# Kernel tuning notes

Measured on AMD Instinct MI355X. Metric: run time of the kernel, lower is better.

Reference implementation:

```python
import jax, jax.numpy as jnp
import numpy as np

B, T, D, H = 4, 2048, 1024, 16
HD = D // H
SCALE = D ** (-0.5)  # note: module scales by d_model**-0.5, not head_dim**-0.5


def setup_inputs() -> dict:
    key = jax.random.key(0)
    k1, k2, k3 = jax.random.split(key, 3)
    x = jax.random.normal(k1, (B, T, D), dtype=jnp.float32)
    Wqkv = jax.random.normal(k2, (D, 3 * D), dtype=jnp.float32) * (D ** -0.5)
    Wo = jax.random.normal(k3, (D, D), dtype=jnp.float32) * (D ** -0.5)
    return {"x": x, "Wqkv": Wqkv, "Wo": Wo}


def reference(x, Wqkv, Wo):
    b, t, c = x.shape
    qkv = x @ Wqkv  # [B,T,3D]
    q, k, v = jnp.split(qkv, 3, axis=-1)
    q = q.reshape(b, t, H, HD).transpose(0, 2, 1, 3)  # [B,H,T,HD]
    k = k.reshape(b, t, H, HD).transpose(0, 2, 1, 3)
    v = v.reshape(b, t, H, HD).transpose(0, 2, 1, 3)
    attn = jnp.einsum('bhid,bhjd->bhij', q, k) * SCALE  # [B,H,T,T]
    mask = jnp.tril(jnp.ones((t, t), dtype=jnp.bool_))
    attn = jnp.where(mask[None, None], attn, jnp.finfo(attn.dtype).min)
    attn = jax.nn.softmax(attn, axis=-1)
    out = jnp.einsum('bhij,bhjd->bhid', attn, v)  # [B,H,T,HD]
    out = out.transpose(0, 2, 1, 3).reshape(b, t, c)
    return out @ Wo
```

## Files before the change

### kernel.cpp

```cpp
#include <hip/hip_runtime.h>
#include <hip/hip_bf16.h>

#define B_ 4
#define T_ 2048
#define D_ 1024
#define H_ 16
#define HD_ 64

typedef __bf16 bf16;
typedef __bf16 bf16x8 __attribute__((ext_vector_type(8)));
typedef __bf16 bf16x4 __attribute__((ext_vector_type(4)));
typedef float f32x4 __attribute__((ext_vector_type(4)));
typedef float f32x16 __attribute__((ext_vector_type(16)));

#define MFMA16(a, b, c) __builtin_amdgcn_mfma_f32_16x16x32_bf16(a, b, c, 0, 0, 0)
#define MFMA32(a, b, c) __builtin_amdgcn_mfma_f32_32x32x16_bf16(a, b, c, 0, 0, 0)

__device__ inline void gld_lds16(const bf16* g, bf16* l) {
  __builtin_amdgcn_global_load_lds((const __attribute__((address_space(1))) void*)g,
                                   (__attribute__((address_space(3))) void*)l, 16, 0, 0);
}

__device__ inline unsigned pkbf16(float a, float b) {
  unsigned r;
  asm("v_cvt_pk_bf16_f32 %0, %1, %2" : "=v"(r) : "v"(a), "v"(b));
  return r;
}
__device__ inline void pl32swap(unsigned& x, unsigned& y) {
  asm("v_permlane32_swap_b32 %0, %1" : "+v"(x), "+v"(y));
}

#define PACKJ(dst, S, base)                        \
  {                                                \
    unsigned w0 = pkbf16(S[base + 0], S[base + 1]); \
    unsigned w2 = pkbf16(S[base + 4], S[base + 5]); \
    pl32swap(w0, w2);                              \
    unsigned w1 = pkbf16(S[base + 2], S[base + 3]); \
    unsigned w3 = pkbf16(S[base + 6], S[base + 7]); \
    pl32swap(w1, w3);                              \
    int4 wi = {(int)w0, (int)w1, (int)w2, (int)w3}; \
    dst = __builtin_bit_cast(bf16x8, wi);          \
  }

__global__ void cvt_f32_bf16(const float* __restrict__ in, bf16* __restrict__ out) {
  int i = (blockIdx.x * 256 + threadIdx.x) * 8;
  float4 v0 = *(const float4*)(in + i);
  float4 v1 = *(const float4*)(in + i + 4);
  bf16x8 o = {(bf16)v0.x, (bf16)v0.y, (bf16)v0.z, (bf16)v0.w,
              (bf16)v1.x, (bf16)v1.y, (bf16)v1.z, (bf16)v1.w};
  *(bf16x8*)(out + i) = o;
}

__global__ void transpose_f32_bf16(const float* __restrict__ in, bf16* __restrict__ out,
                                   int R, int C) {
  __shared__ float tile[32][33];
  int c0 = blockIdx.x * 32, r0 = blockIdx.y * 32;
  int tx = threadIdx.x, ty = threadIdx.y;
#pragma unroll
  for (int i = 0; i < 4; i++)
    tile[ty + i * 8][tx] = in[(size_t)(r0 + ty + i * 8) * C + c0 + tx];
  __syncthreads();
#pragma unroll
  for (int i = 0; i < 4; i++)
    out[(size_t)(c0 + ty + i * 8) * R + r0 + tx] = (bf16)tile[tx][ty + i * 8];
}

__global__ __launch_bounds__(512) void gemm_qkv(const bf16* __restrict__ A,
                                                const bf16* __restrict__ Bt,
                                                bf16* __restrict__ qb, bf16* __restrict__ kb,
                                                bf16* __restrict__ vtb, int M, int N, int K) {
  __shared__ __align__(16) bf16 lds_a[2][256 * 32];
  __shared__ __align__(16) bf16 lds_b[2][128 * 32];
  int bid = blockIdx.x;
  int m0 = ((bid & 7) * 4 + ((bid >> 3) & 3)) * 256;
  int n0 = (bid >> 5) * 128;
  int tid = threadIdx.x, wave = tid >> 6, lane = tid & 63;
  int l16 = lane & 15, lhi = lane >> 4;
  int wr = wave >> 1, wc = wave & 1;
  f32x4 acc[4][4];
#pragma unroll
  for (int mt = 0; mt < 4; mt++)
#pragma unroll
    for (int nt = 0; nt < 4; nt++) acc[mt][nt] = (f32x4){0.f, 0.f, 0.f, 0.f};

  int scol = (lane & 3) * 8;
  const bf16* ga0 = A + (size_t)(m0 + wave * 32 + (lane >> 2)) * K + scol;
  const bf16* ga1 = ga0 + (size_t)16 * K;
  const bf16* gb = Bt + (size_t)(n0 + wave * 16 + (lane >> 2)) * K + scol;

  auto STAGE = [&](int buf, int k0) {
    gld_lds16(ga0 + k0, &lds_a[buf][wave * 1024]);
    gld_lds16(ga1 + k0, &lds_a[buf][wave * 1024 + 512]);
    gld_lds16(gb + k0, &lds_b[buf][wave * 512]);
  };

  int NT = K >> 5;
  STAGE(0, 0);
  STAGE(1, 32);
  for (int t = 0; t < NT; t++) {
    if (t + 1 < NT)
      asm volatile("s_waitcnt vmcnt(3)" ::: "memory");
    else
      asm volatile("s_waitcnt vmcnt(0)" ::: "memory");
    __builtin_amdgcn_s_barrier();
    const bf16* la = lds_a[t & 1];
    const bf16* lb = lds_b[t & 1];
    bf16x8 af[4], bfr[4];
#pragma unroll
    for (int mt = 0; mt < 4; mt++)
      af[mt] = *(const bf16x8*)&la[(wr * 64 + mt * 16 + l16) * 32 + 8 * lhi];
#pragma unroll
    for (int nt = 0; nt < 4; nt++)
      bfr[nt] = *(const bf16x8*)&lb[(wc * 64 + nt * 16 + l16) * 32 + 8 * lhi];
    asm volatile("s_waitcnt lgkmcnt(0)" ::: "memory");
    __builtin_amdgcn_s_barrier();
    if (t + 2 < NT) STAGE(t & 1, (t + 2) * 32);
    __builtin_amdgcn_s_setprio(1);
#pragma unroll
    for (int mt = 0; mt < 4; mt++)
#pragma unroll
      for (int nt = 0; nt < 4; nt++) acc[mt][nt] = MFMA16(af[mt], bfr[nt], acc[mt][nt]);
    __builtin_amdgcn_s_setprio(0);
  }

  __syncthreads();
  int col0 = n0 + wc * 64;
  int sec = col0 >> 10;
  int h = (col0 & 1023) >> 6;
  float scale = (sec == 0) ? 0.045084439f : 1.f;
  bf16* scr = ((bf16*)lds_a) + wave * 1168;
#pragma unroll
  for (int mt = 0; mt < 4; mt++) {
#pragma unroll
    for (int nt = 0; nt < 4; nt++)
#pragma unroll
      for (int rr = 0; rr < 4; rr++)
        scr[(4 * lhi + rr) * 72 + nt * 16 + l16] = (bf16)(acc[mt][nt][rr] * scale);
    int row0 = m0 + wr * 64 + mt * 16;
    int b = row0 >> 11, tt0 = row0 & (T_ - 1);
    if (sec != 2) {
      bf16* dst = (sec == 0) ? qb : kb;
#pragma unroll
      for (int p = 0; p < 2; p++) {
        int r16 = p * 8 + (lane >> 3);
        int c8 = (lane & 7) * 8;
        bf16x8 v = *(const bf16x8*)(scr + r16 * 72 + c8);
        *(bf16x8*)(dst + ((size_t)(b * H_ + h) * T_ + tt0 + r16) * HD_ + c8) = v;
      }
    } else {
      int d = lane;
      bf16x8 v0, v1;
#pragma unroll
      for (int e = 0; e < 8; e++) {
        v0[e] = scr[e * 72 + d];
        v1[e] = scr[(8 + e) * 72 + d];
      }
      bf16* vt = vtb + ((size_t)(b * H_ + h) * HD_ + d) * T_ + tt0;
      *(bf16x8*)(vt) = v0;
      *(bf16x8*)(vt + 8) = v1;
    }
  }
}

__global__ __launch_bounds__(256) void gemm_out(const bf16* __restrict__ A,
                                                const bf16* __restrict__ Bt,
                                                float* __restrict__ fout, int M, int N, int K) {
  __shared__ __align__(16) bf16 lds_a[2][128 * 32];
  __shared__ __align__(16) bf16 lds_b[2][128 * 32];
  int bid = blockIdx.x;
  int m0 = ((bid & 7) * 8 + ((bid >> 3) & 7)) * 128;
  int n0 = (bid >> 6) * 128;
  int tid = threadIdx.x, wave = tid >> 6, lane = tid & 63;
  int l16 = lane & 15, lhi = lane >> 4;
  int wr = wave >> 1, wc = wave & 1;
  f32x4 acc[4][4];
#pragma unroll
  for (int mt = 0; mt < 4; mt++)
#pragma unroll
    for (int nt = 0; nt < 4; nt++) acc[mt][nt] = (f32x4){0.f, 0.f, 0.f, 0.f};

  int sr = wave * 16 + (lane >> 2);
  int scol = (lane & 3) * 8;
  const bf16* ga = A + (size_t)(m0 + sr) * K + scol;
  const bf16* gb = Bt + (size_t)(n0 + sr) * K + scol;

  auto STAGE = [&](int buf, int k0) {
    gld_lds16(ga + k0, &lds_a[buf][wave * 512]);
    gld_lds16(ga + (size_t)64 * K + k0, &lds_a[buf][2048 + wave * 512]);
    gld_lds16(gb + k0, &lds_b[buf][wave * 512]);
    gld_lds16(gb + (size_t)64 * K + k0, &lds_b[buf][2048 + wave * 512]);
  };

  int NT = K >> 5;
  STAGE(0, 0);
  STAGE(1, 32);
  for (int t = 0; t < NT; t++) {
    if (t + 1 < NT)
      asm volatile("s_waitcnt vmcnt(4)" ::: "memory");
    else
      asm volatile("s_waitcnt vmcnt(0)" ::: "memory");
    __builtin_amdgcn_s_barrier();
    const bf16* la = lds_a[t & 1];
    const bf16* lb = lds_b[t & 1];
    bf16x8 af[4], bfr[4];
#pragma unroll
    for (int mt = 0; mt < 4; mt++)
      af[mt] = *(const bf16x8*)&la[(wr * 64 + mt * 16 + l16) * 32 + 8 * lhi];
#pragma unroll
    for (int nt = 0; nt < 4; nt++)
      bfr[nt] = *(const bf16x8*)&lb[(wc * 64 + nt * 16 + l16) * 32 + 8 * lhi];
    asm volatile("s_waitcnt lgkmcnt(0)" ::: "memory");
    __builtin_amdgcn_s_barrier();
    if (t + 2 < NT) STAGE(t & 1, (t + 2) * 32);
    __builtin_amdgcn_s_setprio(1);
#pragma unroll
    for (int mt = 0; mt < 4; mt++)
#pragma unroll
      for (int nt = 0; nt < 4; nt++) acc[mt][nt] = MFMA16(af[mt], bfr[nt], acc[mt][nt]);
    __builtin_amdgcn_s_setprio(0);
  }

#pragma unroll
  for (int mt = 0; mt < 4; mt++)
#pragma unroll
    for (int nt = 0; nt < 4; nt++)
#pragma unroll
      for (int rr = 0; rr < 4; rr++) {
        int row = m0 + wr * 64 + mt * 16 + 4 * lhi + rr;
        int col = n0 + wc * 64 + nt * 16 + l16;
        fout[(size_t)row * N + col] = acc[mt][nt][rr];
      }
}

__global__ __launch_bounds__(256, 4) void attn_kernel(const bf16* __restrict__ qbuf,
                                                      const bf16* __restrict__ kbuf,
                                                      const bf16* __restrict__ vtbuf,
                                                      bf16* __restrict__ obuf) {
  __shared__ __align__(16) bf16 sm[16384];
  int bid = blockIdx.x;
  int bh = (bid & 7) * 8 + ((bid >> 3) & 7);
  const int qtab[16] = {15, 14, 13, 12, 8, 9, 10, 11, 6, 4, 5, 7, 1, 3, 2, 0};
  int qi = qtab[bid >> 6];
  int q0 = qi * 128;
  int wv = threadIdx.x >> 6;
  int lane = threadIdx.x & 63;
  int q = lane & 31, hi = lane >> 5;
  int qw = q0 + wv * 32;
  int b = bh >> 4, h = bh & 15;

  const bf16* Q = qbuf + (size_t)bh * T_ * HD_;
  const bf16* Kg = kbuf + (size_t)bh * T_ * HD_;
  const bf16* Vt = vtbuf + (size_t)bh * HD_ * T_;

  bf16x8 qf[4];
#pragma unroll
  for (int j = 0; j < 4; j++)
    qf[j] = *(const bf16x8*)(Q + (size_t)(qw + q) * HD_ + j * 16 + hi * 8);

  int srow = lane >> 3;
  int sc8 = ((lane & 7) ^ srow) * 8;
  int r0 = wv * 16;
  const bf16* kgp = Kg + (size_t)(r0 + srow) * HD_ + sc8;
  const bf16* vgp = Vt + (size_t)(r0 + srow) * T_ + sc8;

  auto stage = [&](int buf, int t) {
    const bf16* kg = kgp + (size_t)t * 64 * HD_;
    const bf16* vg = vgp + t * 64;
    bf16* kd = sm + buf * 4096;
    bf16* vd = sm + 8192 + buf * 4096;
    gld_lds16(kg, kd + r0 * 64);
    gld_lds16(kg + 8 * HD_, kd + (r0 + 8) * 64);
    gld_lds16(vg, vd + r0 * 64);
    gld_lds16(vg + 8 * T_, vd + (r0 + 8) * 64);
  };

  int xo = (q & 7) << 4;
  int A0 = q * 128 + ((16 * hi) ^ xo);
  int A1 = q * 128 + ((32 + 16 * hi) ^ xo);
  int A2 = q * 128 + ((64 + 16 * hi) ^ xo);
  int A3 = q * 128 + ((96 + 16 * hi) ^ xo);
  const char* smc = (const char*)sm;

  f32x16 o1, o2;
#pragma unroll
  for (int r = 0; r < 16; r++) {
    o1[r] = 0.f;
    o2[r] = 0.f;
  }
  f32x16 zro;
#pragma unroll
  for (int r = 0; r < 16; r++) zro[r] = 0.f;
  float l_r = 0.f;
  const float MFIX = 12.f;
  int ntm = 2 * qi + 2;

  stage(0, 0);
  stage(1, 1);
  for (int t = 0; t < ntm; ++t) {
    if (t + 1 < ntm)
      asm volatile("s_waitcnt vmcnt(4)" ::: "memory");
    else
      asm volatile("s_waitcnt vmcnt(0)" ::: "memory");
    __builtin_amdgcn_s_barrier();
    int KB = (t & 1) * 8192;
    int VB = 16384 + (t & 1) * 8192;
    int jb = t * 64;
    bool active = (jb <= qw + 31);
    bf16x8 pf0, pf1, pf2, pf3;
    bf16x8 vf0, vf1, vf2, vf3, vf4, vf5, vf6, vf7;
    if (active) {
      bf16x8 kf[8];
      kf[0] = *(const bf16x8*)(smc + KB + A0);
      kf[1] = *(const bf16x8*)(smc + KB + A1);
      kf[2] = *(const bf16x8*)(smc + KB + A2);
      kf[3] = *(const bf16x8*)(smc + KB + A3);
      kf[4] = *(const bf16x8*)(smc + KB + 4096 + A0);
      kf[5] = *(const bf16x8*)(smc + KB + 4096 + A1);
      kf[6] = *(const bf16x8*)(smc + KB + 4096 + A2);
      kf[7] = *(const bf16x8*)(smc + KB + 4096 + A3);
      f32x16 s1, s2;
      __builtin_amdgcn_s_setprio(1);
      s1 = MFMA32(kf[0], qf[0], zro);
#pragma unroll
      for (int j = 1; j < 4; j++) s1 = MFMA32(kf[j], qf[j], s1);
      s2 = MFMA32(kf[4], qf[0], zro);
#pragma unroll
      for (int j = 1; j < 4; j++) s2 = MFMA32(kf[4 + j], qf[j], s2);
      __builtin_amdgcn_s_setprio(0);
      if (jb + 63 > qw) {
#pragma unroll
        for (int r = 0; r < 16; r++) {
          int kv = (r & 3) + 8 * (r >> 2) + 4 * hi;
          if (jb + kv > qw + q) s1[r] = -1e30f;
          if (jb + kv + 32 > qw + q) s2[r] = -1e30f;
        }
      }
#pragma unroll
      for (int r = 0; r < 16; r++) s1[r] = exp2f(s1[r] - MFIX);
#pragma unroll
      for (int r = 0; r < 16; r++) s2[r] = exp2f(s2[r] - MFIX);
      float ts[8];
#pragma unroll
      for (int r = 0; r < 8; r++) ts[r] = (s1[r] + s1[r + 8]) + (s2[r] + s2[r + 8]);
#pragma unroll
      for (int r = 0; r < 4; r++) ts[r] += ts[r + 4];
      float su = (ts[0] + ts[1]) + (ts[2] + ts[3]);
      su += __shfl_xor(su, 32);
      l_r += su;
      PACKJ(pf0, s1, 0);
      PACKJ(pf1, s1, 8);
      PACKJ(pf2, s2, 0);
      PACKJ(pf3, s2, 8);
      vf0 = *(const bf16x8*)(smc + VB + A0);
      vf1 = *(const bf16x8*)(smc + VB + A1);
      vf2 = *(const bf16x8*)(smc + VB + A2);
      vf3 = *(const bf16x8*)(smc + VB + A3);
      vf4 = *(const bf16x8*)(smc + VB + 4096 + A0);
      vf5 = *(const bf16x8*)(smc + VB + 4096 + A1);
      vf6 = *(const bf16x8*)(smc + VB + 4096 + A2);
      vf7 = *(const bf16x8*)(smc + VB + 4096 + A3);
    }
    asm volatile("s_waitcnt lgkmcnt(0)" ::: "memory");
    __builtin_amdgcn_s_barrier();
    if (t + 2 < ntm) stage(t & 1, t + 2);
    if (active) {
      __builtin_amdgcn_s_setprio(1);
      o1 = MFMA32(vf0, pf0, o1);
      o2 = MFMA32(vf4, pf0, o2);
      o1 = MFMA32(vf1, pf1, o1);
      o2 = MFMA32(vf5, pf1, o2);
      o1 = MFMA32(vf2, pf2, o1);
      o2 = MFMA32(vf6, pf2, o2);
      o1 = MFMA32(vf3, pf3, o1);
      o2 = MFMA32(vf7, pf3, o2);
      __builtin_amdgcn_s_setprio(0);
    }
  }
  __syncthreads();

  bf16* scr = sm + wv * 2112;
  float inv = 1.f / l_r;
#pragma unroll
  for (int r = 0; r < 16; r++) {
    int d = (r & 3) + 8 * (r >> 2) + 4 * hi;
    scr[d * 33 + q] = (bf16)(o1[r] * inv);
    scr[(32 + d) * 33 + q] = (bf16)(o2[r] * inv);
  }
#pragma unroll
  for (int pass = 0; pass < 4; pass++) {
    int row = qw + pass * 8 + (lane >> 3);
    int dcol = (lane & 7) * 8;
    bf16x8 ov;
#pragma unroll
    for (int e = 0; e < 8; e++) ov[e] = scr[(dcol + e) * 33 + pass * 8 + (lane >> 3)];
    *(bf16x8*)(obuf + ((size_t)(b * T_ + row)) * D_ + h * 64 + dcol) = ov;
  }
}

extern "C" void kernel_launch(void* const* d_in, const int* in_sizes, int n_in, void* d_out,
                              int out_size, void* d_ws, size_t ws_size, hipStream_t stream) {
  const float* x = (const float*)d_in[0];
  const float* wqkv = (const float*)d_in[1];
  const float* wo = (const float*)d_in[2];
  float* out = (float*)d_out;
  char* ws = (char*)d_ws;

  bf16* xb = (bf16*)ws;
  bf16* wqkvt = (bf16*)(ws + (16u << 20));
  bf16* wot = (bf16*)(ws + (22u << 20));
  bf16* qb = (bf16*)(ws + (24u << 20));
  bf16* kb = (bf16*)(ws + (40u << 20));
  bf16* vtb = (bf16*)(ws + (72u << 20));
  bf16* ao = (bf16*)(ws + (88u << 20));

  cvt_f32_bf16<<<4096, 256, 0, stream>>>(x, xb);
  transpose_f32_bf16<<<dim3(96, 32), dim3(32, 8), 0, stream>>>(wqkv, wqkvt, 1024, 3072);
  transpose_f32_bf16<<<dim3(32, 32), dim3(32, 8), 0, stream>>>(wo, wot, 1024, 1024);
  gemm_qkv<<<768, 512, 0, stream>>>(xb, wqkvt, qb, kb, vtb, B_ * T_, 3 * D_, D_);
  attn_kernel<<<1024, 256, 0, stream>>>(qb, kb, vtb, ao);
  gemm_out<<<512, 256, 0, stream>>>(ao, wot, out, B_ * T_, D_, D_);
}
```

Baseline: 170.3 us.

## Fuse prep kernels into one launch and shrink QKV GEMM tile to 128x128

Merges the x conversion and the two weight transposes into a single prep kernel that dispatches on block index, removing two kernel launches and their gaps. The QKV GEMM changes from 256x128 tiles with 512 threads to 128x128 tiles with 256 threads and 1536 blocks, with the staging and vmcnt wait counts updated to match. The aim is lower launch overhead and better occupancy and load balance across CUs. The cost is less data reuse per tile, since more blocks re-read the A and B operands.

```diff
diff --git a/kernel.cpp b/kernel.cpp
--- a/kernel.cpp
+++ b/kernel.cpp
@@ -9,7 +9,6 @@
 
 typedef __bf16 bf16;
 typedef __bf16 bf16x8 __attribute__((ext_vector_type(8)));
-typedef __bf16 bf16x4 __attribute__((ext_vector_type(4)));
 typedef float f32x4 __attribute__((ext_vector_type(4)));
 typedef float f32x16 __attribute__((ext_vector_type(16)));
 
@@ -42,20 +41,11 @@
     dst = __builtin_bit_cast(bf16x8, wi);          \
   }
 
-__global__ void cvt_f32_bf16(const float* __restrict__ in, bf16* __restrict__ out) {
-  int i = (blockIdx.x * 256 + threadIdx.x) * 8;
-  float4 v0 = *(const float4*)(in + i);
-  float4 v1 = *(const float4*)(in + i + 4);
-  bf16x8 o = {(bf16)v0.x, (bf16)v0.y, (bf16)v0.z, (bf16)v0.w,
-              (bf16)v1.x, (bf16)v1.y, (bf16)v1.z, (bf16)v1.w};
-  *(bf16x8*)(out + i) = o;
-}
-
-__global__ void transpose_f32_bf16(const float* __restrict__ in, bf16* __restrict__ out,
-                                   int R, int C) {
+__device__ inline void tr_body(const float* __restrict__ in, bf16* __restrict__ out, int R,
+                               int C, int bx, int by, int tid) {
   __shared__ float tile[32][33];
-  int c0 = blockIdx.x * 32, r0 = blockIdx.y * 32;
-  int tx = threadIdx.x, ty = threadIdx.y;
+  int c0 = bx * 32, r0 = by * 32;
+  int tx = tid & 31, ty = tid >> 5;
 #pragma unroll
   for (int i = 0; i < 4; i++)
     tile[ty + i * 8][tx] = in[(size_t)(r0 + ty + i * 8) * C + c0 + tx];
@@ -65,15 +55,37 @@
     out[(size_t)(c0 + ty + i * 8) * R + r0 + tx] = (bf16)tile[tx][ty + i * 8];
 }
 
-__global__ __launch_bounds__(512) void gemm_qkv(const bf16* __restrict__ A,
+__global__ __launch_bounds__(256) void prep(const float* __restrict__ x, bf16* __restrict__ xb,
+                                            const float* __restrict__ wqkv,
+                                            bf16* __restrict__ wqkvt,
+                                            const float* __restrict__ wo,
+                                            bf16* __restrict__ wot) {
+  int bid = blockIdx.x;
+  if (bid < 4096) {
+    int i = (bid * 256 + threadIdx.x) * 8;
+    float4 v0 = *(const float4*)(x + i);
+    float4 v1 = *(const float4*)(x + i + 4);
+    bf16x8 o = {(bf16)v0.x, (bf16)v0.y, (bf16)v0.z, (bf16)v0.w,
+                (bf16)v1.x, (bf16)v1.y, (bf16)v1.z, (bf16)v1.w};
+    *(bf16x8*)(xb + i) = o;
+  } else if (bid < 7168) {
+    int u = bid - 4096;
+    tr_body(wqkv, wqkvt, 1024, 3072, u % 96, u / 96, threadIdx.x);
+  } else {
+    int u = bid - 7168;
+    tr_body(wo, wot, 1024, 1024, u & 31, u >> 5, threadIdx.x);
+  }
+}
+
+__global__ __launch_bounds__(256) void gemm_qkv(const bf16* __restrict__ A,
                                                 const bf16* __restrict__ Bt,
                                                 bf16* __restrict__ qb, bf16* __restrict__ kb,
                                                 bf16* __restrict__ vtb, int M, int N, int K) {
-  __shared__ __align__(16) bf16 lds_a[2][256 * 32];
+  __shared__ __align__(16) bf16 lds_a[2][128 * 32];
   __shared__ __align__(16) bf16 lds_b[2][128 * 32];
   int bid = blockIdx.x;
-  int m0 = ((bid & 7) * 4 + ((bid >> 3) & 3)) * 256;
-  int n0 = (bid >> 5) * 128;
+  int m0 = ((bid & 7) * 8 + ((bid >> 3) & 7)) * 128;
+  int n0 = (bid >> 6) * 128;
   int tid = threadIdx.x, wave = tid >> 6, lane = tid & 63;
   int l16 = lane & 15, lhi = lane >> 4;
   int wr = wave >> 1, wc = wave & 1;
@@ -83,15 +95,16 @@
 #pragma unroll
     for (int nt = 0; nt < 4; nt++) acc[mt][nt] = (f32x4){0.f, 0.f, 0.f, 0.f};
 
+  int sr = wave * 16 + (lane >> 2);
   int scol = (lane & 3) * 8;
-  const bf16* ga0 = A + (size_t)(m0 + wave * 32 + (lane >> 2)) * K + scol;
-  const bf16* ga1 = ga0 + (size_t)16 * K;
-  const bf16* gb = Bt + (size_t)(n0 + wave * 16 + (lane >> 2)) * K + scol;
+  const bf16* ga = A + (size_t)(m0 + sr) * K + scol;
+  const bf16* gb = Bt + (size_t)(n0 + sr) * K + scol;
 
   auto STAGE = [&](int buf, int k0) {
-    gld_lds16(ga0 + k0, &lds_a[buf][wave * 1024]);
-    gld_lds16(ga1 + k0, &lds_a[buf][wave * 1024 + 512]);
+    gld_lds16(ga + k0, &lds_a[buf][wave * 512]);
+    gld_lds16(ga + (size_t)64 * K + k0, &lds_a[buf][2048 + wave * 512]);
     gld_lds16(gb + k0, &lds_b[buf][wave * 512]);
+    gld_lds16(gb + (size_t)64 * K + k0, &lds_b[buf][2048 + wave * 512]);
   };
 
   int NT = K >> 5;
@@ -99,7 +112,7 @@
   STAGE(1, 32);
   for (int t = 0; t < NT; t++) {
     if (t + 1 < NT)
-      asm volatile("s_waitcnt vmcnt(3)" ::: "memory");
+      asm volatile("s_waitcnt vmcnt(4)" ::: "memory");
     else
       asm volatile("s_waitcnt vmcnt(0)" ::: "memory");
     __builtin_amdgcn_s_barrier();
@@ -413,10 +426,8 @@
   bf16* vtb = (bf16*)(ws + (72u << 20));
   bf16* ao = (bf16*)(ws + (88u << 20));
 
-  cvt_f32_bf16<<<4096, 256, 0, stream>>>(x, xb);
-  transpose_f32_bf16<<<dim3(96, 32), dim3(32, 8), 0, stream>>>(wqkv, wqkvt, 1024, 3072);
-  transpose_f32_bf16<<<dim3(32, 32), dim3(32, 8), 0, stream>>>(wo, wot, 1024, 1024);
-  gemm_qkv<<<768, 512, 0, stream>>>(xb, wqkvt, qb, kb, vtb, B_ * T_, 3 * D_, D_);
+  prep<<<8192, 256, 0, stream>>>(x, xb, wqkv, wqkvt, wo, wot);
+  gemm_qkv<<<1536, 256, 0, stream>>>(xb, wqkvt, qb, kb, vtb, B_ * T_, 3 * D_, D_);
   attn_kernel<<<1024, 256, 0, stream>>>(qb, kb, vtb, ao);
   gemm_out<<<512, 256, 0, stream>>>(ao, wot, out, B_ * T_, D_, D_);
 }
```

New measurement: 165.8 us. -2.6%, faster.
